# Optimization experiments

Hardware: AMD Instinct MI355X
Metric: run time of the kernel (lower is better)

The kernel has to match this reference:

```python
import jax, jax.numpy as jnp
import numpy as np

B, C, H, W = 8, 96, 224, 224
OUT = 2 * C  # BatchNorm2d(in_channels*2) forces out_channels == 2*in_channels
BN_EPS = 1e-5


def setup_inputs() -> dict:
    key = jax.random.key(0)
    ks = jax.random.split(key, 6)
    x = jax.random.normal(ks[0], (B, C, H, W), dtype=jnp.float32)
    # 1x1 conv: weight [OUT, 2C], bias [OUT]
    conv_w = jax.random.normal(ks[1], (OUT, 2 * C), dtype=jnp.float32) * (2 * C) ** -0.5
    conv_b = jax.random.normal(ks[2], (OUT,), dtype=jnp.float32) * 0.01
    # BatchNorm2d(2C) in eval mode: gamma, beta, running mean/var
    bn_gamma = jnp.ones((OUT,), dtype=jnp.float32)
    bn_beta = jnp.zeros((OUT,), dtype=jnp.float32)
    bn_mean = jax.random.normal(ks[3], (OUT,), dtype=jnp.float32) * 0.01
    bn_var = jax.random.uniform(ks[4], (OUT,), dtype=jnp.float32, minval=0.5, maxval=1.5)
    return {"x": x, "conv_w": conv_w, "conv_b": conv_b,
            "bn_gamma": bn_gamma, "bn_beta": bn_beta,
            "bn_mean": bn_mean, "bn_var": bn_var}


def reference(x, conv_w, conv_b, bn_gamma, bn_beta, bn_mean, bn_var):
    d = C ** -0.5
    # gather strided superpatch nodes
    sel = x[:, :, ::4, ::4]                      # [B, C, h, w]
    b, c, h, w = sel.shape
    q = sel.reshape(b, c, h * w).transpose(0, 2, 1)  # [B, hw, C]
    # dense self-attention on superpatch tokens (q == k == v)
    att = jax.nn.softmax(jnp.einsum('bnc,bmc->bnm', q, q) * d, axis=-1)
    att = jnp.einsum('bnm,bmc->bnc', att, q)     # [B, hw, C]
    att = att.transpose(0, 2, 1).reshape(b, c, h, w)
    # nearest-neighbor upsample back to [H, W] (scatter)
    att = jnp.repeat(jnp.repeat(att, 4, axis=2), 4, axis=3)  # [B, C, H, W]
    # concat + 1x1 conv + BN(eval) + GELU(exact erf)
    cat = jnp.concatenate([x, att], axis=1)      # [B, 2C, H, W]
    y = jnp.einsum('bchw,oc->bohw', cat, conv_w) + conv_b[None, :, None, None]
    inv_std = jax.lax.rsqrt(bn_var + BN_EPS)
    y = (y - bn_mean[None, :, None, None]) * (inv_std * bn_gamma)[None, :, None, None] + bn_beta[None, :, None, None]
    return jax.nn.gelu(y, approximate=False)
```

## Files before the change

### kernel.cpp

```cpp
#include <hip/hip_runtime.h>
#include <math.h>

constexpr int Bn  = 8;
constexpr int Cn  = 96;
constexpr int Hn  = 224;
constexpr int Wn  = 224;
constexpr int HWn = Hn * Wn;
constexpr int Nn  = 56 * 56;
constexpr int On  = 192;

typedef unsigned short u16;
typedef __attribute__((ext_vector_type(8))) short bfrag;
typedef __attribute__((ext_vector_type(4))) float f32x4;

__device__ inline u16 f2b(float f) {
  unsigned int u = __float_as_uint(f);
  u += 0x7fffu + ((u >> 16) & 1u);
  return (u16)(u >> 16);
}

__device__ inline float gelu_f(float v) {
  float u2 = v * fmaf(0.0713548162f, v * v, 1.5957691216f);
  u2 = fminf(fmaxf(u2, -80.f), 80.f);
  float e = __expf(u2);
  return v * e * __builtin_amdgcn_rcpf(e + 1.0f);
}

__global__ __launch_bounds__(256) void k_build_q16(const float* __restrict__ x,
                                                   u16* __restrict__ qb) {
  int idx = blockIdx.x * 256 + threadIdx.x;
  int c = idx % Cn;
  int t = idx / Cn;
  int n = t % Nn;
  int b = t / Nn;
  int hp = n / 56, wp = n - hp * 56;
  qb[idx] = f2b(x[((b * Cn + c) * Hn + hp * 4) * Wn + wp * 4]);
}

__global__ __launch_bounds__(256) void k_wt16(const float* __restrict__ w,
                                              u16* __restrict__ wb) {
  int idx = blockIdx.x * 256 + threadIdx.x;
  wb[idx] = f2b(w[idx]);
}

__global__ __launch_bounds__(256) void k_flash(const u16* __restrict__ qb,
                                               float* __restrict__ part) {
  __shared__ __align__(16) char smem[18944];
  u16* ksm = (u16*)smem;
  u16* pl  = (u16*)(smem + 14336);
  float* ored = (float*)smem;

  const int tid  = threadIdx.x;
  const int lane = tid & 63;
  const int wid  = tid >> 6;
  const int r = lane & 15, g = lane >> 4;
  const int wq = wid & 1, wk = wid >> 1;
  const int tile = blockIdx.x, b = blockIdx.y, kseg = blockIdx.z;
  const float scale = 0.10206207262f;

  const int tbeg = kseg * 12;
  const int tend = (kseg == 3) ? 49 : (kseg + 1) * 12;

  if (tid < 64) {
    int m = tid;
    int base = ((m >> 2) * 7 + 6) * 64 + (m & 3) * 16;
    uint4 a0 = {0x00003F80u, 0u, 0u, 0u};
    uint4 z0 = {0u, 0u, 0u, 0u};
    *(uint4*)&ksm[base] = a0;
    *(uint4*)&ksm[base + 8] = z0;
  }

  const u16* qp = qb + (size_t)(b * Nn + tile * 32 + wq * 16 + r) * Cn;
  bfrag aq[3];
#pragma unroll
  for (int ks = 0; ks < 3; ++ks) aq[ks] = *(const bfrag*)(qp + ks * 32 + g * 8);

  f32x4 of[7];
#pragma unroll
  for (int i = 0; i < 7; ++i) of[i] = (f32x4){0.f, 0.f, 0.f, 0.f};

  const uint4* q16 = (const uint4*)(qb + (size_t)b * Nn * Cn);

  const int vbase = (wk * 8 + g * 2) * 896 + 8 * r;

  for (int ti = tbeg; ti < tend; ++ti) {
    __syncthreads();
#pragma unroll
    for (int i = 0; i < 3; ++i) {
      int f = tid + i * 256;
      int row = f / 12, cb = f - row * 12;
      uint4 v = q16[(size_t)(ti * 64 + row) * 12 + cb];
      int off = ((row >> 2) * 7 + (cb >> 1)) * 64 + (row & 3) * 16 + (cb & 1) * 8;
      *(uint4*)&ksm[off] = v;
    }
    __syncthreads();

    f32x4 s0 = {0.f, 0.f, 0.f, 0.f}, s1 = {0.f, 0.f, 0.f, 0.f};
    const int mc0 = wk * 32 + r, mc1 = mc0 + 16;
#pragma unroll
    for (int ks = 0; ks < 3; ++ks) {
      int o0 = ((mc0 >> 2) * 7 + ks * 2 + (g >> 1)) * 64 + (mc0 & 3) * 16 + (g & 1) * 8;
      int o1 = ((mc1 >> 2) * 7 + ks * 2 + (g >> 1)) * 64 + (mc1 & 3) * 16 + (g & 1) * 8;
      bfrag bk0 = *(const bfrag*)&ksm[o0];
      bfrag bk1 = *(const bfrag*)&ksm[o1];
      s0 = __builtin_amdgcn_mfma_f32_16x16x32_bf16(aq[ks], bk0, s0, 0, 0, 0);
      s1 = __builtin_amdgcn_mfma_f32_16x16x32_bf16(aq[ks], bk1, s1, 0, 0, 0);
    }

#pragma unroll
    for (int reg = 0; reg < 4; ++reg) {
      int prow = wq * 16 + 4 * g + reg;
      pl[prow * 72 + wk * 32 + r]      = f2b(__expf(s0[reg] * scale));
      pl[prow * 72 + wk * 32 + 16 + r] = f2b(__expf(s1[reg] * scale));
    }

    uint2 trv[7][2];
#pragma unroll
    for (int nf = 0; nf < 7; ++nf) {
#pragma unroll
      for (int tt = 0; tt < 2; ++tt) {
        int ab = vbase + tt * 896 + nf * 128;
        asm volatile("ds_read_b64_tr_b16 %0, %1" : "=v"(trv[nf][tt]) : "v"(ab));
      }
    }
    bfrag pa = *(const bfrag*)&pl[(wq * 16 + r) * 72 + wk * 32 + g * 8];
    asm volatile("s_waitcnt lgkmcnt(0)" ::: "memory");
    __builtin_amdgcn_sched_barrier(0);
#pragma unroll
    for (int nf = 0; nf < 7; ++nf) {
      union { bfrag f; uint2 u[2]; } cv;
      cv.u[0] = trv[nf][0];
      cv.u[1] = trv[nf][1];
      of[nf] = __builtin_amdgcn_mfma_f32_16x16x32_bf16(pa, cv.f, of[nf], 0, 0, 0);
    }
  }

  __syncthreads();
  if (wk == 1) {
    int base = (wq * 64 + lane) * 28;
#pragma unroll
    for (int nf = 0; nf < 7; ++nf)
#pragma unroll
      for (int reg = 0; reg < 4; ++reg) ored[base + nf * 4 + reg] = of[nf][reg];
  }
  __syncthreads();
  if (wk == 0) {
    int base = (wq * 64 + lane) * 28;
#pragma unroll
    for (int nf = 0; nf < 7; ++nf)
#pragma unroll
      for (int reg = 0; reg < 4; ++reg) of[nf][reg] += ored[base + nf * 4 + reg];
    float* pb = part + ((size_t)(kseg * Bn + b) * Nn) * 104;
    const int row0 = tile * 32 + wq * 16 + 4 * g;
#pragma unroll
    for (int reg = 0; reg < 4; ++reg) {
      float* pr = pb + (size_t)(row0 + reg) * 104;
#pragma unroll
      for (int nf = 0; nf < 6; ++nf) pr[nf * 16 + r] = of[nf][reg];
      if (r == 0) pr[96] = of[6][reg];
    }
  }
}

__global__ __launch_bounds__(256) void k_red(const float* __restrict__ part,
                                             u16* __restrict__ attP) {
  int idx = blockIdx.x * 256 + threadIdx.x;
  int c4 = idx % 24;
  int bn = idx / 24;
  constexpr size_t SEG = (size_t)Bn * Nn * 104;
  const float* p0 = part + (size_t)bn * 104;
  float4 s = {0.f, 0.f, 0.f, 0.f};
  float d = 0.f;
#pragma unroll
  for (int ks = 0; ks < 4; ++ks) {
    const float* p = p0 + ks * SEG;
    float4 v = *(const float4*)(p + c4 * 4);
    s.x += v.x; s.y += v.y; s.z += v.z; s.w += v.w;
    d += p[96];
  }
  float inv = 1.0f / d;
  uint2 o;
  o.x = (unsigned)f2b(s.x * inv) | ((unsigned)f2b(s.y * inv) << 16);
  o.y = (unsigned)f2b(s.z * inv) | ((unsigned)f2b(s.w * inv) << 16);
  *(uint2*)(attP + (size_t)bn * 96 + c4 * 4) = o;
}

__global__ __launch_bounds__(256, 3) void k_convmma(
    const float* __restrict__ x, const u16* __restrict__ attP,
    const u16* __restrict__ wb, const float* __restrict__ cvb,
    const float* __restrict__ gam, const float* __restrict__ bet,
    const float* __restrict__ mu, const float* __restrict__ va,
    float* __restrict__ out) {
  __shared__ u16 ldsT[96 * 68];
  __shared__ u16 ldsA[64 * 100];
  __shared__ u16 ldsV[16 * 104];

  const int tid  = threadIdx.x;
  const int lane = tid & 63;
  const int wid  = tid >> 6;
  const int r = lane & 15, g = lane >> 4;
  const int ow = wid * 48;
  const int tile = blockIdx.x;
  const int p0 = tile * 64;

  bfrag wf[3][6];
#pragma unroll
  for (int of = 0; of < 3; ++of)
#pragma unroll
    for (int ks = 0; ks < 6; ++ks)
      wf[of][ks] = *(const bfrag*)(wb + (ow + of * 16 + r) * On + ks * 32 + g * 8);

  float scv[3], shv[3];
#pragma unroll
  for (int of = 0; of < 3; ++of) {
    int o = ow + of * 16 + r;
    float s = rsqrtf(va[o] + 1e-5f) * gam[o];
    scv[of] = s;
    shv[of] = (cvb[o] - mu[o]) * s + bet[o];
  }

  const int nn_t = tid / 12, cbn = tid - nn_t * 12;
  int natt = 0;
  if (tid < 192) {
    int p = p0 + nn_t * 4;
    int h = p / Wn, w = p - h * Wn;
    natt = (h >> 2) * 56 + (w >> 2);
  }

  const float4* x4 = (const float4*)x;

  for (int b = blockIdx.y * 2; b < (int)blockIdx.y * 2 + 2; ++b) {
    __syncthreads();
#pragma unroll
    for (int i = 0; i < 6; ++i) {
      int f = tid + i * 256;
      int c = f >> 4, q4 = f & 15;
      float4 v = x4[((size_t)(b * Cn + c) * HWn + p0) / 4 + q4];
      uint2 pk;
      pk.x = (unsigned)f2b(v.x) | ((unsigned)f2b(v.y) << 16);
      pk.y = (unsigned)f2b(v.z) | ((unsigned)f2b(v.w) << 16);
      *(uint2*)&ldsT[c * 68 + q4 * 4] = pk;
    }
    if (tid < 192) {
      uint4 v = *(const uint4*)(attP + ((size_t)b * Nn + natt) * Cn + cbn * 8);
      *(uint4*)&ldsV[nn_t * 104 + cbn * 8] = v;
    }
    __syncthreads();
    {
      const int px = tid >> 2, sub = tid & 3;
      uint wbuf[12];
#pragma unroll
      for (int i = 0; i < 12; ++i) {
        unsigned e0 = ldsT[(sub * 24 + 2 * i) * 68 + px];
        unsigned e1 = ldsT[(sub * 24 + 2 * i + 1) * 68 + px];
        wbuf[i] = e0 | (e1 << 16);
      }
#pragma unroll
      for (int i = 0; i < 3; ++i)
        *(uint4*)&ldsA[px * 100 + sub * 24 + i * 8] = *(uint4*)&wbuf[i * 4];
    }
    __syncthreads();
    f32x4 acc[4][3];
#pragma unroll
    for (int pf = 0; pf < 4; ++pf)
#pragma unroll
      for (int of = 0; of < 3; ++of) acc[pf][of] = (f32x4){0.f, 0.f, 0.f, 0.f};

#pragma unroll
    for (int ks = 0; ks < 6; ++ks) {
#pragma unroll
      for (int pf = 0; pf < 4; ++pf) {
        bfrag a;
        if (ks < 3) a = *(const bfrag*)&ldsA[(pf * 16 + r) * 100 + ks * 32 + g * 8];
        else        a = *(const bfrag*)&ldsV[(pf * 4 + (r >> 2)) * 104 + (ks - 3) * 32 + g * 8];
#pragma unroll
        for (int of = 0; of < 3; ++of)
          acc[pf][of] = __builtin_amdgcn_mfma_f32_16x16x32_bf16(a, wf[of][ks], acc[pf][of], 0, 0, 0);
      }
    }
#pragma unroll
    for (int of = 0; of < 3; ++of) {
      const size_t obase = ((size_t)b * On + ow + of * 16 + r) * (size_t)HWn + p0;
#pragma unroll
      for (int pf = 0; pf < 4; ++pf) {
        float4 o4;
        float* po = (float*)&o4;
#pragma unroll
        for (int reg = 0; reg < 4; ++reg) {
          float v = fmaf(acc[pf][of][reg], scv[of], shv[of]);
          po[reg] = gelu_f(v);
        }
        *reinterpret_cast<float4*>(out + obase + pf * 16 + 4 * g) = o4;
      }
    }
  }
}

extern "C" void kernel_launch(void* const* d_in, const int* in_sizes, int n_in,
                              void* d_out, int out_size, void* d_ws, size_t ws_size,
                              hipStream_t stream) {
  const float* x      = (const float*)d_in[0];
  const float* conv_w = (const float*)d_in[1];
  const float* conv_b = (const float*)d_in[2];
  const float* gam    = (const float*)d_in[3];
  const float* bet    = (const float*)d_in[4];
  const float* mu     = (const float*)d_in[5];
  const float* va     = (const float*)d_in[6];
  float* out = (float*)d_out;

  char* ws = (char*)d_ws;
  constexpr size_t QB16 = (size_t)Bn * Nn * Cn * sizeof(u16);
  u16* qb16 = (u16*)(ws);
  u16* attP = (u16*)(ws + QB16);
  u16* wb16 = (u16*)(ws + 2 * QB16);

  float* part = out;

  k_build_q16<<<dim3((Bn * Nn * Cn) / 256), dim3(256), 0, stream>>>(x, qb16);
  k_wt16     <<<dim3((On * On) / 256),      dim3(256), 0, stream>>>(conv_w, wb16);
  k_flash    <<<dim3(98, Bn, 4), dim3(256), 0, stream>>>(qb16, part);
  k_red      <<<dim3((Bn * Nn * 24) / 256), dim3(256), 0, stream>>>(part, attP);
  k_convmma  <<<dim3(784, 4), dim3(256), 0, stream>>>(x, attP, wb16, conv_b, gam, bet, mu, va, out);
}
```

Baseline: 281.7 us.

## Use LDS transpose reads to drop the explicit LDS transpose pass in conv kernel

The x tile is now stored in LDS in a blocked 4x4 layout, and the MFMA A-fragments are read with ds_read_b64_tr_b16, which transposes as it loads. This removes the separate transpose pass, one __syncthreads, and the second LDS buffer. The smaller LDS footprint lets launch bounds rise to 4 blocks per CU. The risks are that the inline asm relies on gfx950 transpose-read semantics being correct, and that the explicit lgkmcnt wait plus sched_barrier limit how well loads and MFMAs overlap.

```diff
diff --git a/kernel.cpp b/kernel.cpp
--- a/kernel.cpp
+++ b/kernel.cpp
@@ -185,15 +185,15 @@
   *(uint2*)(attP + (size_t)bn * 96 + c4 * 4) = o;
 }
 
-__global__ __launch_bounds__(256, 3) void k_convmma(
+__global__ __launch_bounds__(256, 4) void k_convmma(
     const float* __restrict__ x, const u16* __restrict__ attP,
     const u16* __restrict__ wb, const float* __restrict__ cvb,
     const float* __restrict__ gam, const float* __restrict__ bet,
     const float* __restrict__ mu, const float* __restrict__ va,
     float* __restrict__ out) {
-  __shared__ u16 ldsT[96 * 68];
-  __shared__ u16 ldsA[64 * 100];
-  __shared__ u16 ldsV[16 * 104];
+  __shared__ __align__(16) char csm[15616];
+  u16* ldsX = (u16*)csm;
+  u16* ldsV = (u16*)(csm + 12288);
 
   const int tid  = threadIdx.x;
   const int lane = tid & 63;
@@ -228,6 +228,7 @@
   }
 
   const float4* x4 = (const float4*)x;
+  const int abase = 8 * r;
 
   for (int b = blockIdx.y * 2; b < (int)blockIdx.y * 2 + 2; ++b) {
     __syncthreads();
@@ -239,27 +240,15 @@
       uint2 pk;
       pk.x = (unsigned)f2b(v.x) | ((unsigned)f2b(v.y) << 16);
       pk.y = (unsigned)f2b(v.z) | ((unsigned)f2b(v.w) << 16);
-      *(uint2*)&ldsT[c * 68 + q4 * 4] = pk;
+      int off = ((c >> 2) * 4 + (q4 >> 2)) * 64 + (c & 3) * 16 + (q4 & 3) * 4;
+      *(uint2*)&ldsX[off] = pk;
     }
     if (tid < 192) {
       uint4 v = *(const uint4*)(attP + ((size_t)b * Nn + natt) * Cn + cbn * 8);
       *(uint4*)&ldsV[nn_t * 104 + cbn * 8] = v;
     }
     __syncthreads();
-    {
-      const int px = tid >> 2, sub = tid & 3;
-      uint wbuf[12];
-#pragma unroll
-      for (int i = 0; i < 12; ++i) {
-        unsigned e0 = ldsT[(sub * 24 + 2 * i) * 68 + px];
-        unsigned e1 = ldsT[(sub * 24 + 2 * i + 1) * 68 + px];
-        wbuf[i] = e0 | (e1 << 16);
-      }
-#pragma unroll
-      for (int i = 0; i < 3; ++i)
-        *(uint4*)&ldsA[px * 100 + sub * 24 + i * 8] = *(uint4*)&wbuf[i * 4];
-    }
-    __syncthreads();
+
     f32x4 acc[4][3];
 #pragma unroll
     for (int pf = 0; pf < 4; ++pf)
@@ -267,17 +256,38 @@
       for (int of = 0; of < 3; ++of) acc[pf][of] = (f32x4){0.f, 0.f, 0.f, 0.f};
 
 #pragma unroll
-    for (int ks = 0; ks < 6; ++ks) {
+    for (int ks = 0; ks < 3; ++ks) {
+      uint2 ta[4][2];
 #pragma unroll
       for (int pf = 0; pf < 4; ++pf) {
-        bfrag a;
-        if (ks < 3) a = *(const bfrag*)&ldsA[(pf * 16 + r) * 100 + ks * 32 + g * 8];
-        else        a = *(const bfrag*)&ldsV[(pf * 4 + (r >> 2)) * 104 + (ks - 3) * 32 + g * 8];
+        int ab0 = ((ks * 8 + g * 2) * 4 + pf) * 128 + abase;
+        int ab1 = ab0 + 512;
+        asm volatile("ds_read_b64_tr_b16 %0, %1" : "=v"(ta[pf][0]) : "v"(ab0));
+        asm volatile("ds_read_b64_tr_b16 %0, %1" : "=v"(ta[pf][1]) : "v"(ab1));
+      }
+      asm volatile("s_waitcnt lgkmcnt(0)" ::: "memory");
+      __builtin_amdgcn_sched_barrier(0);
+#pragma unroll
+      for (int pf = 0; pf < 4; ++pf) {
+        union { bfrag f; uint2 u[2]; } cv;
+        cv.u[0] = ta[pf][0];
+        cv.u[1] = ta[pf][1];
+#pragma unroll
+        for (int of = 0; of < 3; ++of)
+          acc[pf][of] = __builtin_amdgcn_mfma_f32_16x16x32_bf16(cv.f, wf[of][ks], acc[pf][of], 0, 0, 0);
+      }
+    }
+#pragma unroll
+    for (int ks = 3; ks < 6; ++ks) {
+#pragma unroll
+      for (int pf = 0; pf < 4; ++pf) {
+        bfrag a = *(const bfrag*)&ldsV[(pf * 4 + (r >> 2)) * 104 + (ks - 3) * 32 + g * 8];
 #pragma unroll
         for (int of = 0; of < 3; ++of)
           acc[pf][of] = __builtin_amdgcn_mfma_f32_16x16x32_bf16(a, wf[of][ks], acc[pf][of], 0, 0, 0);
       }
     }
+
 #pragma unroll
     for (int of = 0; of < 3; ++of) {
       const size_t obase = ((size_t)b * On + ow + of * 16 + r) * (size_t)HWn + p0;
```

Result: slower. 337.3 us (+19.7%).

## Prefetch next batch's x and attention tiles into registers in conv kernel

Applied to the files above, without the earlier changes.

The conv+BN+GELU kernel now handles four batches per block instead of two, launching half as many blocks in y. It loads the next batch's x and attention tiles into registers while the current batch is converted and computed, so global loads overlap the MMA work. Launch bounds are raised to 4 waves per SIMD to improve occupancy, which adds register pressure alongside the prefetch registers. Flash partial sums now go to the workspace when it is large enough instead of the output buffer.

```diff
diff --git a/kernel.cpp b/kernel.cpp
--- a/kernel.cpp
+++ b/kernel.cpp
@@ -185,7 +185,7 @@
   *(uint2*)(attP + (size_t)bn * 96 + c4 * 4) = o;
 }
 
-__global__ __launch_bounds__(256, 3) void k_convmma(
+__global__ __launch_bounds__(256, 4) void k_convmma(
     const float* __restrict__ x, const u16* __restrict__ attP,
     const u16* __restrict__ wb, const float* __restrict__ cvb,
     const float* __restrict__ gam, const float* __restrict__ bet,
@@ -228,22 +228,36 @@
   }
 
   const float4* x4 = (const float4*)x;
-
-  for (int b = blockIdx.y * 2; b < (int)blockIdx.y * 2 + 2; ++b) {
+  const int cT = tid >> 4, q4T = tid & 15;
+
+  const int b0 = blockIdx.y * 4;
+
+  float4 xr[6];
+  uint4  ar;
+
+#pragma unroll
+  for (int i = 0; i < 6; ++i)
+    xr[i] = x4[((size_t)(b0 * Cn + cT + i * 16) * HWn + p0) / 4 + q4T];
+  if (tid < 192)
+    ar = *(const uint4*)(attP + ((size_t)b0 * Nn + natt) * Cn + cbn * 8);
+
+  for (int bi = 0; bi < 4; ++bi) {
+    const int b = b0 + bi;
     __syncthreads();
 #pragma unroll
     for (int i = 0; i < 6; ++i) {
-      int f = tid + i * 256;
-      int c = f >> 4, q4 = f & 15;
-      float4 v = x4[((size_t)(b * Cn + c) * HWn + p0) / 4 + q4];
       uint2 pk;
-      pk.x = (unsigned)f2b(v.x) | ((unsigned)f2b(v.y) << 16);
-      pk.y = (unsigned)f2b(v.z) | ((unsigned)f2b(v.w) << 16);
-      *(uint2*)&ldsT[c * 68 + q4 * 4] = pk;
-    }
-    if (tid < 192) {
-      uint4 v = *(const uint4*)(attP + ((size_t)b * Nn + natt) * Cn + cbn * 8);
-      *(uint4*)&ldsV[nn_t * 104 + cbn * 8] = v;
+      pk.x = (unsigned)f2b(xr[i].x) | ((unsigned)f2b(xr[i].y) << 16);
+      pk.y = (unsigned)f2b(xr[i].z) | ((unsigned)f2b(xr[i].w) << 16);
+      *(uint2*)&ldsT[(cT + i * 16) * 68 + q4T * 4] = pk;
+    }
+    if (tid < 192) *(uint4*)&ldsV[nn_t * 104 + cbn * 8] = ar;
+    if (bi < 3) {
+#pragma unroll
+      for (int i = 0; i < 6; ++i)
+        xr[i] = x4[((size_t)((b + 1) * Cn + cT + i * 16) * HWn + p0) / 4 + q4T];
+      if (tid < 192)
+        ar = *(const uint4*)(attP + ((size_t)(b + 1) * Nn + natt) * Cn + cbn * 8);
     }
     __syncthreads();
     {
@@ -314,11 +328,14 @@
   u16* attP = (u16*)(ws + QB16);
   u16* wb16 = (u16*)(ws + 2 * QB16);
 
-  float* part = out;
+  constexpr size_t PART_OFF   = 16u << 20;
+  constexpr size_t PART_BYTES = (size_t)4 * Bn * Nn * 104 * 4;
+  float* part = (ws_size >= PART_OFF + PART_BYTES) ? (float*)(ws + PART_OFF)
+                                                   : out;
 
   k_build_q16<<<dim3((Bn * Nn * Cn) / 256), dim3(256), 0, stream>>>(x, qb16);
   k_wt16     <<<dim3((On * On) / 256),      dim3(256), 0, stream>>>(conv_w, wb16);
   k_flash    <<<dim3(98, Bn, 4), dim3(256), 0, stream>>>(qb16, part);
   k_red      <<<dim3((Bn * Nn * 24) / 256), dim3(256), 0, stream>>>(part, attP);
-  k_convmma  <<<dim3(784, 4), dim3(256), 0, stream>>>(x, attP, wb16, conv_b, gam, bet, mu, va, out);
-}
+  k_convmma  <<<dim3(784, 2), dim3(256), 0, stream>>>(x, attP, wb16, conv_b, gam, bet, mu, va, out);
+}
```

Measured after the change: 320.4 us. +13.7%, slower.
